# Kernel tuning notes

Hardware: AMD Instinct MI355X
Metric: run time of the kernel (lower is better)

The kernel has to match this reference:

```python
import jax, jax.numpy as jnp
import numpy as np
import math

B, S, D, H = 2048, 32, 1024, 16
DK = D // H
EPS = 1e-5

def setup_inputs() -> dict:
    key = jax.random.key(0)
    ks = jax.random.split(key, 8)
    w_scale = 0.02  # realistic init scale for linear weights
    # Weights stored as (d_in, d_out): y = x @ W + b (same math as torch x @ W.T)
    return {
        "x":  jax.random.normal(ks[0], (B, S, D), jnp.float32),
        "ln_g": jnp.ones((D,), jnp.float32),
        "ln_b": jnp.zeros((D,), jnp.float32),
        "wq": jax.random.normal(ks[1], (D, D), jnp.float32) * w_scale,
        "bq": jnp.zeros((D,), jnp.float32),
        "wk": jax.random.normal(ks[2], (D, D), jnp.float32) * w_scale,
        "bk": jnp.zeros((D,), jnp.float32),
        "wv": jax.random.normal(ks[3], (D, D), jnp.float32) * w_scale,
        "bv": jnp.zeros((D,), jnp.float32),
        "wo": jax.random.normal(ks[4], (D, D), jnp.float32) * w_scale,
        "bo": jnp.zeros((D,), jnp.float32),
        "rel_bias": jax.random.normal(ks[5], (H, 32, 32), jnp.float32),
    }

def reference(x, ln_g, ln_b, wq, bq, wk, bk, wv, bv, wo, bo, rel_bias):
    b, s, d = x.shape
    h = rel_bias.shape[0]
    dk = d // h
    residual = x
    # LayerNorm (eps=1e-5)
    mu = jnp.mean(x, axis=-1, keepdims=True)
    var = jnp.mean(jnp.square(x - mu), axis=-1, keepdims=True)
    xn = (x - mu) * jax.lax.rsqrt(var + EPS) * ln_g + ln_b
    # QKV projections -> [b, h, s, dk]
    def split_heads(t):
        return t.reshape(b, s, h, dk).transpose(0, 2, 1, 3)
    Q = split_heads(xn @ wq + bq)
    K = split_heads(xn @ wk + bk)
    V = split_heads(xn @ wv + bv)
    scores = jnp.einsum('bhqd,bhkd->bhqk', Q, K) / jnp.sqrt(jnp.float32(dk))
    if s <= 32:  # static at trace time, matching the torch branch
        scores = scores + rel_bias[:, :s, :s][None]
    attn = jax.nn.softmax(scores, axis=-1)
    ctx = jnp.einsum('bhqk,bhkd->bhqd', attn, V)
    ctx = ctx.transpose(0, 2, 1, 3).reshape(b, s, d)
    out = ctx @ wo + bo  # dropout is identity in eval
    return residual + out
```

## Files before the change

### kernel.cpp

```cpp
#include <hip/hip_runtime.h>
#include <stdint.h>


typedef __attribute__((ext_vector_type(8))) short bf16x8;
typedef __attribute__((ext_vector_type(4))) float f32x4;
typedef __attribute__((ext_vector_type(16))) float f32x16;

__device__ __forceinline__ float bf2f(unsigned short u) {
    return __uint_as_float(((unsigned)u) << 16);
}
__device__ __forceinline__ unsigned short f2bf(float f) {
    unsigned u = __float_as_uint(f);
    u += 0x7FFFu + ((u >> 16) & 1u);
    return (unsigned short)(u >> 16);
}
__device__ __forceinline__ uint4 pack8(const float* f) {
    uint4 u;
    u.x = (unsigned)f2bf(f[0]) | ((unsigned)f2bf(f[1]) << 16);
    u.y = (unsigned)f2bf(f[2]) | ((unsigned)f2bf(f[3]) << 16);
    u.z = (unsigned)f2bf(f[4]) | ((unsigned)f2bf(f[5]) << 16);
    u.w = (unsigned)f2bf(f[6]) | ((unsigned)f2bf(f[7]) << 16);
    return u;
}

typedef __attribute__((address_space(3))) unsigned lds_u32;
typedef const __attribute__((address_space(1))) unsigned glb_u32;
__device__ __forceinline__ void gld16(const void* g, void* l) {
    __builtin_amdgcn_global_load_lds((glb_u32*)g, (lds_u32*)l, 16, 0, 0);
}

__global__ __launch_bounds__(256) void lnw_kernel(
    const float* __restrict__ x, const float* __restrict__ gg,
    const float* __restrict__ bb, unsigned short* __restrict__ xn,
    const float* __restrict__ wq, const float* __restrict__ wk,
    const float* __restrict__ wv, const float* __restrict__ wo,
    unsigned short* __restrict__ wcatT, unsigned short* __restrict__ woT)
{
    __shared__ unsigned short T[64 * 72];
    if (blockIdx.x >= 16384) {
        int bid = blockIdx.x - 16384;
        int p = bid >> 8;
        int t = bid & 255;
        int k0 = (t >> 4) * 64, n0 = (t & 15) * 64;
        const float* src = (p == 0) ? wq : (p == 1) ? wk : (p == 2) ? wv : wo;
        unsigned short* dst = (p < 3) ? (wcatT + (size_t)p * 1048576) : woT;
        int tid = threadIdx.x;
#pragma unroll
        for (int it = 0; it < 2; it++) {
            int flat = it * 2048 + tid * 8;
            int r = flat >> 6, c = flat & 63;
            const float* s4 = src + (size_t)(k0 + r) * 1024 + n0 + c;
            float4 u0 = *(const float4*)s4;
            float4 u1 = *(const float4*)(s4 + 4);
            float f[8] = {u0.x, u0.y, u0.z, u0.w, u1.x, u1.y, u1.z, u1.w};
            *(uint4*)&T[r * 72 + c] = pack8(f);
        }
        __syncthreads();
#pragma unroll
        for (int it = 0; it < 2; it++) {
            int flat = it * 2048 + tid * 8;
            int rn = flat >> 6, ck = flat & 63;
            unsigned short v[8];
#pragma unroll
            for (int j = 0; j < 8; j++) v[j] = T[(ck + j) * 72 + rn];
            uint4 u;
            u.x = (unsigned)v[0] | ((unsigned)v[1] << 16);
            u.y = (unsigned)v[2] | ((unsigned)v[3] << 16);
            u.z = (unsigned)v[4] | ((unsigned)v[5] << 16);
            u.w = (unsigned)v[6] | ((unsigned)v[7] << 16);
            *(uint4*)(dst + (size_t)(n0 + rn) * 1024 + k0 + ck) = u;
        }
        return;
    }
    int l = threadIdx.x & 63;
    size_t row = (size_t)blockIdx.x * 4 + (threadIdx.x >> 6);
    const float* xr = x + row * 1024;
    float f0[8], f1[8];
    *(float4*)&f0[0] = *(const float4*)(xr + l * 8);
    *(float4*)&f0[4] = *(const float4*)(xr + l * 8 + 4);
    *(float4*)&f1[0] = *(const float4*)(xr + 512 + l * 8);
    *(float4*)&f1[4] = *(const float4*)(xr + 512 + l * 8 + 4);
    float s = 0.f, s2 = 0.f;
#pragma unroll
    for (int j = 0; j < 8; j++) { s += f0[j] + f1[j]; s2 += f0[j] * f0[j] + f1[j] * f1[j]; }
#pragma unroll
    for (int m = 1; m < 64; m <<= 1) { s += __shfl_xor(s, m); s2 += __shfl_xor(s2, m); }
    float mu = s * (1.f / 1024.f);
    float var = s2 * (1.f / 1024.f) - mu * mu;
    float rs = rsqrtf(var + 1e-5f);
    float fg0[8], fg1[8], fb0[8], fb1[8];
    *(float4*)&fg0[0] = *(const float4*)(gg + l * 8);
    *(float4*)&fg0[4] = *(const float4*)(gg + l * 8 + 4);
    *(float4*)&fg1[0] = *(const float4*)(gg + 512 + l * 8);
    *(float4*)&fg1[4] = *(const float4*)(gg + 512 + l * 8 + 4);
    *(float4*)&fb0[0] = *(const float4*)(bb + l * 8);
    *(float4*)&fb0[4] = *(const float4*)(bb + l * 8 + 4);
    *(float4*)&fb1[0] = *(const float4*)(bb + 512 + l * 8);
    *(float4*)&fb1[4] = *(const float4*)(bb + 512 + l * 8 + 4);
    float o0[8], o1[8];
#pragma unroll
    for (int j = 0; j < 8; j++) {
        o0[j] = (f0[j] - mu) * rs * fg0[j] + fb0[j];
        o1[j] = (f1[j] - mu) * rs * fg1[j] + fb1[j];
    }
    *(uint4*)(xn + row * 1024 + l * 8) = pack8(o0);
    *(uint4*)(xn + row * 1024 + 512 + l * 8) = pack8(o1);
}

#define FENCE asm volatile("" ::: "memory")
#define BARRIER do { FENCE; __builtin_amdgcn_s_barrier(); FENCE; } while (0)
#define WAIT_LGKM0 do { asm volatile("s_waitcnt lgkmcnt(0)" ::: "memory"); \
                        __builtin_amdgcn_sched_barrier(0); } while (0)
#define VMCNT(n) asm volatile("s_waitcnt vmcnt(" #n ")" ::: "memory")

#define SAp(buf) (LDSU + (buf) * 16384)
#define SBp(buf) (LDSU + 32768 + (buf) * 16384)

#define STG(gb, hh, kcol, ldsreg) do { \
    const unsigned short* _g = (gb) + (size_t)((hh) * 128) * 1024 + (kcol); \
    unsigned short* _d = (ldsreg) + ((hh) * 128 + w * 8) * 64; \
    gld16(_g, _d); gld16(_g + 64 * 1024, _d + 64 * 64); } while (0)

#define LDA(buf, q, rfq, ks) (*(const bf16x8*)&SAp(buf)[ \
    (wm * 128 + (q) * 32 + (rfq) * 16 + (l & 15)) * 64 + ((((ks) * 32) + khi) ^ aswz)])
#define LDB(buf, cf, ks) (*(const bf16x8*)&SBp(buf)[ \
    (wn * 64 + (cf) * 16 + (l & 15)) * 64 + ((((ks) * 32) + khi) ^ aswz)])

#define MFMA_QUAD(q) do { \
    _Pragma("unroll") \
    for (int cf = 0; cf < 4; cf++) { \
        acc[(q)*2+0][cf] = __builtin_amdgcn_mfma_f32_16x16x32_bf16(aF00, bF[cf][0], acc[(q)*2+0][cf], 0, 0, 0); \
        acc[(q)*2+0][cf] = __builtin_amdgcn_mfma_f32_16x16x32_bf16(aF01, bF[cf][1], acc[(q)*2+0][cf], 0, 0, 0); \
        acc[(q)*2+1][cf] = __builtin_amdgcn_mfma_f32_16x16x32_bf16(aF10, bF[cf][0], acc[(q)*2+1][cf], 0, 0, 0); \
        acc[(q)*2+1][cf] = __builtin_amdgcn_mfma_f32_16x16x32_bf16(aF11, bF[cf][1], acc[(q)*2+1][cf], 0, 0, 0); \
    } } while (0)

#define PHASE(buf, q, STAGE_STMT, TAIL_STMT) do { \
    bf16x8 aF00 = LDA(buf, q, 0, 0), aF01 = LDA(buf, q, 0, 1); \
    bf16x8 aF10 = LDA(buf, q, 1, 0), aF11 = LDA(buf, q, 1, 1); \
    if ((q) == 0) { \
        _Pragma("unroll") \
        for (int cf = 0; cf < 4; cf++) { bF[cf][0] = LDB(buf, cf, 0); bF[cf][1] = LDB(buf, cf, 1); } \
    } \
    STAGE_STMT; \
    BARRIER; \
    WAIT_LGKM0; \
    __builtin_amdgcn_s_setprio(1); \
    MFMA_QUAD(q); \
    __builtin_amdgcn_s_setprio(0); \
    TAIL_STMT; \
    BARRIER; \
} while (0)

template <int MODE>
__global__ __launch_bounds__(512, 2) void gemm8(
    const unsigned short* __restrict__ A, const unsigned short* __restrict__ Bt,
    const float* __restrict__ bz0, const float* __restrict__ bz1,
    const float* __restrict__ bz2, const float* __restrict__ resid,
    void* __restrict__ outv, int NTL, size_t pstride)
{
    __shared__ __align__(16) unsigned short LDSU[65536];
    int cpx = gridDim.x >> 3;
    int bid = (blockIdx.x & 7) * cpx + (blockIdx.x >> 3);
    int mt = bid / NTL, ntl = bid % NTL;
    int m0 = mt * 256, n0 = ntl * 256;
    int tid = threadIdx.x, l = tid & 63, w = tid >> 6;
    int wm = w >> 2, wn = w & 3;
    int khi = (l >> 4) * 8;
    int aswz = (l & 7) * 8;

    const unsigned short* Ag = A + (size_t)(m0 + w * 8 + (l >> 3)) * 1024 + ((l & 7) ^ (l >> 3)) * 8;
    const unsigned short* Bg = Bt + (size_t)(n0 + w * 8 + (l >> 3)) * 1024 + ((l & 7) ^ (l >> 3)) * 8;
    unsigned short* sA0 = SAp(0);
    unsigned short* sA1 = SAp(1);
    unsigned short* sB0 = SBp(0);
    unsigned short* sB1 = SBp(1);

    f32x4 acc[8][4];
#pragma unroll
    for (int i = 0; i < 8; i++)
#pragma unroll
        for (int j = 0; j < 4; j++)
#pragma unroll
            for (int v = 0; v < 4; v++) acc[i][j][v] = 0.f;

    bf16x8 bF[4][2];

    STG(Ag, 0, 0, sA0); STG(Ag, 1, 0, sA0);
    STG(Bg, 0, 0, sB0); STG(Bg, 1, 0, sB0);
    STG(Bg, 0, 64, sB1); STG(Bg, 1, 64, sB1);
    VMCNT(4);
    BARRIER;

    for (int it = 0; it < 7; ++it) {
        int koff = it * 128;
        PHASE(0, 0, STG(Ag, 0, koff + 64, sA1), (void)0);
        PHASE(0, 1, STG(Ag, 1, koff + 64, sA1), (void)0);
        PHASE(0, 2, STG(Bg, 0, koff + 128, sB0), (void)0);
        PHASE(0, 3, STG(Bg, 1, koff + 128, sB0), VMCNT(4));
        PHASE(1, 0, STG(Ag, 0, koff + 128, sA0), (void)0);
        PHASE(1, 1, STG(Ag, 1, koff + 128, sA0), (void)0);
        PHASE(1, 2, STG(Bg, 0, koff + 192, sB1), (void)0);
        PHASE(1, 3, STG(Bg, 1, koff + 192, sB1), VMCNT(4));
    }
    PHASE(0, 0, STG(Ag, 0, 960, sA1), (void)0);
    PHASE(0, 1, STG(Ag, 1, 960, sA1), (void)0);
    PHASE(0, 2, (void)0, (void)0);
    PHASE(0, 3, (void)0, VMCNT(0));
    PHASE(1, 0, (void)0, (void)0);
    PHASE(1, 1, (void)0, (void)0);
    PHASE(1, 2, (void)0, (void)0);
    PHASE(1, 3, (void)0, (void)0);
    __builtin_amdgcn_sched_barrier(0);

    if (MODE == 0) {
        unsigned short* Cs = LDSU;
        unsigned short* out = (unsigned short*)outv;
        int p = n0 >> 10;
        const float* bp = (p == 0) ? bz0 : (p == 1) ? bz1 : bz2;
        size_t pbase = (size_t)p * pstride;
        __syncthreads();
#pragma unroll
        for (int cf = 0; cf < 4; cf++) {
            int colc = wn * 64 + cf * 16 + (l & 15);
            int nn = ((n0 + colc) & 1023);
            float bias = bp[nn];
            int c8 = colc >> 3, ce = colc & 7;
#pragma unroll
            for (int rf = 0; rf < 8; rf++) {
#pragma unroll
                for (int v = 0; v < 4; v++) {
                    int rloc = wm * 128 + rf * 16 + (l >> 4) * 4 + v;
                    Cs[rloc * 256 + ((c8 ^ (rloc & 7)) << 3) + ce] =
                        f2bf(acc[rf][cf][v] + bias);
                }
            }
        }
        __syncthreads();
        int bg0 = m0 >> 5;
        int hg0 = (n0 & 1023) >> 6;
#pragma unroll
        for (int k = 0; k < 4; k++) {
            int pi = w * 4 + k;
            int b = pi >> 2, hh = pi & 3;
#pragma unroll
            for (int r4 = 0; r4 < 4; r4++) {
                int c = r4 * 64 + l;
                int s = c >> 3, d8 = c & 7;
                int row = b * 32 + s;
                int c8 = hh * 8 + d8;
                uint4 val = *(const uint4*)&Cs[row * 256 + ((c8 ^ (row & 7)) << 3)];
                size_t dst = pbase + (((size_t)((bg0 + b) * 16 + hg0 + hh) * 32 + s) << 6) + d8 * 8;
                *(uint4*)(out + dst) = val;
            }
        }
    } else {
        float* Cf = (float*)LDSU;
        float* out = (float*)outv;
        int gcol = n0 + l * 4;
        float4 bzv = *(const float4*)(bz0 + gcol);
#pragma unroll
        for (int pass = 0; pass < 2; pass++) {
            __syncthreads();
#pragma unroll
            for (int rfq = 0; rfq < 4; rfq++) {
                int rf = pass * 4 + rfq;
#pragma unroll
                for (int cf = 0; cf < 4; cf++) {
                    int c0 = wn * 64 + cf * 16 + (l & 15);
                    int c4 = c0 >> 2, ce = c0 & 3;
#pragma unroll
                    for (int v = 0; v < 4; v++) {
                        int rl = wm * 64 + rfq * 16 + (l >> 4) * 4 + v;
                        Cf[rl * 256 + ((c4 ^ (rl & 7)) << 2) + ce] = acc[rf][cf][v];
                    }
                }
            }
            __syncthreads();
#pragma unroll
            for (int rb4 = 0; rb4 < 4; rb4++) {
                float4 rz[4], cv[4];
#pragma unroll
                for (int k = 0; k < 4; k++) {
                    int rr = (rb4 * 4 + k) * 8 + w;
                    int grow = m0 + (rr & 63) + ((rr >> 6) << 7) + pass * 64;
                    rz[k] = *(const float4*)(resid + (size_t)grow * 1024 + gcol);
                }
#pragma unroll
                for (int k = 0; k < 4; k++) {
                    int rr = (rb4 * 4 + k) * 8 + w;
                    cv[k] = *(const float4*)&Cf[rr * 256 + ((l ^ (rr & 7)) << 2)];
                }
#pragma unroll
                for (int k = 0; k < 4; k++) {
                    int rr = (rb4 * 4 + k) * 8 + w;
                    int grow = m0 + (rr & 63) + ((rr >> 6) << 7) + pass * 64;
                    float4 o;
                    o.x = cv[k].x + bzv.x + rz[k].x;
                    o.y = cv[k].y + bzv.y + rz[k].y;
                    o.z = cv[k].z + bzv.z + rz[k].z;
                    o.w = cv[k].w + bzv.w + rz[k].w;
                    *(float4*)(out + (size_t)grow * 1024 + gcol) = o;
                }
            }
        }
    }
}

__global__ __launch_bounds__(512) void attn_kernel(
    const unsigned short* __restrict__ qkv, const float* __restrict__ rb,
    unsigned short* __restrict__ ctx, size_t pstride)
{
    __shared__ unsigned short VT[8][64 * 40];
    __shared__ unsigned short Ps[8][32 * 40];
    int w8 = threadIdx.x >> 6, l = threadIdx.x & 63;
    int col = l & 31, hi = l >> 5;
    int bh = blockIdx.x * 8 + w8, h = bh & 15;
    size_t base = (size_t)bh << 11;
    const unsigned short* Qb = qkv + base;
    const unsigned short* Kb = Qb + pstride;
    const unsigned short* Vb = Kb + pstride;
    unsigned short* vt = VT[w8];
    unsigned short* ps = Ps[w8];

#pragma unroll
    for (int r = 0; r < 4; r++) {
        int flat = r * 512 + l * 8;
        int s = flat >> 6, d0 = flat & 63;
        uint4 u = *(const uint4*)(Vb + flat);
        const unsigned short* e = (const unsigned short*)&u;
#pragma unroll
        for (int j = 0; j < 8; j++) vt[(d0 + j) * 40 + s] = e[j];
    }

    f32x16 acc;
#pragma unroll
    for (int i = 0; i < 16; i++) acc[i] = 0.f;
#pragma unroll
    for (int t = 0; t < 4; t++) {
        bf16x8 aQ = *(const bf16x8*)(Qb + col * 64 + t * 16 + hi * 8);
        bf16x8 bK = *(const bf16x8*)(Kb + col * 64 + t * 16 + hi * 8);
        acc = __builtin_amdgcn_mfma_f32_32x32x16_bf16(aQ, bK, acc, 0, 0, 0);
    }

    const float* rbh = rb + h * 1024;
#pragma unroll
    for (int r = 0; r < 16; r++) {
        int m = (r & 3) + 8 * (r >> 2) + 4 * hi;
        float v = acc[r] * 0.125f + rbh[m * 32 + col];
        float mx = v;
#pragma unroll
        for (int msk = 1; msk < 32; msk <<= 1) mx = fmaxf(mx, __shfl_xor(mx, msk));
        float e = __expf(v - mx);
        float sm = e;
#pragma unroll
        for (int msk = 1; msk < 32; msk <<= 1) sm += __shfl_xor(sm, msk);
        ps[m * 40 + col] = f2bf(e / sm);
    }

    bf16x8 pa0 = *(const bf16x8*)&ps[col * 40 + hi * 8];
    bf16x8 pa1 = *(const bf16x8*)&ps[col * 40 + 16 + hi * 8];
    bf16x8 vb00 = *(const bf16x8*)&vt[(col) * 40 + hi * 8];
    bf16x8 vb01 = *(const bf16x8*)&vt[(col) * 40 + 16 + hi * 8];
    bf16x8 vb10 = *(const bf16x8*)&vt[(32 + col) * 40 + hi * 8];
    bf16x8 vb11 = *(const bf16x8*)&vt[(32 + col) * 40 + 16 + hi * 8];
    f32x16 o0, o1;
#pragma unroll
    for (int i = 0; i < 16; i++) { o0[i] = 0.f; o1[i] = 0.f; }
    o0 = __builtin_amdgcn_mfma_f32_32x32x16_bf16(pa0, vb00, o0, 0, 0, 0);
    o0 = __builtin_amdgcn_mfma_f32_32x32x16_bf16(pa1, vb01, o0, 0, 0, 0);
    o1 = __builtin_amdgcn_mfma_f32_32x32x16_bf16(pa0, vb10, o1, 0, 0, 0);
    o1 = __builtin_amdgcn_mfma_f32_32x32x16_bf16(pa1, vb11, o1, 0, 0, 0);

#pragma unroll
    for (int r = 0; r < 16; r++) {
        int m = (r & 3) + 8 * (r >> 2) + 4 * hi;
        vt[m * 72 + col]      = f2bf(o0[r]);
        vt[m * 72 + 32 + col] = f2bf(o1[r]);
    }
    size_t rowb = (size_t)(bh >> 4) * 32;
#pragma unroll
    for (int pass = 0; pass < 4; pass++) {
        int row = pass * 8 + (l >> 3);
        int c = (l & 7) * 8;
        uint4 val = *(const uint4*)&vt[row * 72 + c];
        *(uint4*)(ctx + (rowb + row) * 1024 + h * 64 + c) = val;
    }
}

extern "C" void kernel_launch(void* const* d_in, const int* in_sizes, int n_in,
                              void* d_out, int out_size, void* d_ws, size_t ws_size,
                              hipStream_t stream)
{
    const float* x  = (const float*)d_in[0];
    const float* lg = (const float*)d_in[1];
    const float* lb = (const float*)d_in[2];
    const float* wq = (const float*)d_in[3];
    const float* bq = (const float*)d_in[4];
    const float* wk = (const float*)d_in[5];
    const float* bk = (const float*)d_in[6];
    const float* wv = (const float*)d_in[7];
    const float* bv = (const float*)d_in[8];
    const float* wo = (const float*)d_in[9];
    const float* bo = (const float*)d_in[10];
    const float* rb = (const float*)d_in[11];
    float* out = (float*)d_out;
    unsigned short* ws = (unsigned short*)d_ws;

    unsigned short* wcatT = ws;
    unsigned short* woT   = wcatT + 3145728;
    unsigned short* xnctx = woT + 1048576;
    unsigned short* qkvc  = xnctx + 67108864ull;

    const size_t elems_fixed = 3145728ull + 1048576ull + 67108864ull;
    const size_t need4 = (elems_fixed + 50331648ull) * 2;
    int nChunks = (ws_size >= need4) ? 4 : 8;
    int rowsPer = 65536 / nChunks;
    size_t pstr = (size_t)rowsPer * 1024;

    lnw_kernel<<<dim3(17408), dim3(256), 0, stream>>>(
        x, lg, lb, xnctx, wq, wk, wv, wo, wcatT, woT);

    int gemm0Grid = (rowsPer / 256) * 12;
    int attnGrid  = rowsPer / 16;

    for (int c = 0; c < nChunks; c++) {
        const unsigned short* Ac = xnctx + (size_t)c * pstr;
        unsigned short* ctxc = xnctx + (size_t)c * pstr;
        gemm8<0><<<dim3(gemm0Grid), dim3(512), 0, stream>>>(
            Ac, wcatT, bq, bk, bv, (const float*)nullptr, (void*)qkvc, 12, pstr);
        attn_kernel<<<dim3(attnGrid), dim3(512), 0, stream>>>(qkvc, rb, ctxc, pstr);
    }

    gemm8<1><<<dim3(1024), dim3(512), 0, stream>>>(
        xnctx, woT, bo, bo, bo, x, (void*)out, 4, 0);
}
```

Measured before the change: 800.7 us.

## Run output projection per chunk and prefetch residual before epilogue repack

The output-projection GEMM now launches inside the chunk loop right after each attention kernel, working on that chunk's context and residual slice instead of one large launch at the end. The aim is to keep the context data hot in cache (L2/LLC) between attention and the projection. The epilogue also loads all 16 residual float4 values per pass into registers before the LDS repack and barrier, so global load latency overlaps with the repack. In exchange there are more, smaller launches with smaller grids per chunk, and the larger residual buffer raises register pressure.

```diff
diff --git a/kernel.cpp b/kernel.cpp
--- a/kernel.cpp
+++ b/kernel.cpp
@@ -152,6 +152,22 @@
     BARRIER; \
 } while (0)
 
+#define REPACK(pass) do { \
+    _Pragma("unroll") \
+    for (int rfq = 0; rfq < 4; rfq++) { \
+        int rf = (pass) * 4 + rfq; \
+        _Pragma("unroll") \
+        for (int cf = 0; cf < 4; cf++) { \
+            int c0 = wn * 64 + cf * 16 + (l & 15); \
+            int c4 = c0 >> 2, ce = c0 & 3; \
+            _Pragma("unroll") \
+            for (int v = 0; v < 4; v++) { \
+                int rl = wm * 64 + rfq * 16 + (l >> 4) * 4 + v; \
+                Cf[rl * 256 + ((c4 ^ (rl & 7)) << 2) + ce] = acc[rf][cf][v]; \
+            } \
+        } \
+    } } while (0)
+
 template <int MODE>
 __global__ __launch_bounds__(512, 2) void gemm8(
     const unsigned short* __restrict__ A, const unsigned short* __restrict__ Bt,
@@ -259,50 +275,49 @@
         float* out = (float*)outv;
         int gcol = n0 + l * 4;
         float4 bzv = *(const float4*)(bz0 + gcol);
-#pragma unroll
-        for (int pass = 0; pass < 2; pass++) {
-            __syncthreads();
-#pragma unroll
-            for (int rfq = 0; rfq < 4; rfq++) {
-                int rf = pass * 4 + rfq;
-#pragma unroll
-                for (int cf = 0; cf < 4; cf++) {
-                    int c0 = wn * 64 + cf * 16 + (l & 15);
-                    int c4 = c0 >> 2, ce = c0 & 3;
-#pragma unroll
-                    for (int v = 0; v < 4; v++) {
-                        int rl = wm * 64 + rfq * 16 + (l >> 4) * 4 + v;
-                        Cf[rl * 256 + ((c4 ^ (rl & 7)) << 2) + ce] = acc[rf][cf][v];
-                    }
-                }
-            }
-            __syncthreads();
-#pragma unroll
-            for (int rb4 = 0; rb4 < 4; rb4++) {
-                float4 rz[4], cv[4];
-#pragma unroll
-                for (int k = 0; k < 4; k++) {
-                    int rr = (rb4 * 4 + k) * 8 + w;
-                    int grow = m0 + (rr & 63) + ((rr >> 6) << 7) + pass * 64;
-                    rz[k] = *(const float4*)(resid + (size_t)grow * 1024 + gcol);
-                }
-#pragma unroll
-                for (int k = 0; k < 4; k++) {
-                    int rr = (rb4 * 4 + k) * 8 + w;
-                    cv[k] = *(const float4*)&Cf[rr * 256 + ((l ^ (rr & 7)) << 2)];
-                }
-#pragma unroll
-                for (int k = 0; k < 4; k++) {
-                    int rr = (rb4 * 4 + k) * 8 + w;
-                    int grow = m0 + (rr & 63) + ((rr >> 6) << 7) + pass * 64;
-                    float4 o;
-                    o.x = cv[k].x + bzv.x + rz[k].x;
-                    o.y = cv[k].y + bzv.y + rz[k].y;
-                    o.z = cv[k].z + bzv.z + rz[k].z;
-                    o.w = cv[k].w + bzv.w + rz[k].w;
-                    *(float4*)(out + (size_t)grow * 1024 + gcol) = o;
-                }
-            }
+
+        float4 rzp[16];
+#pragma unroll
+        for (int k = 0; k < 16; k++) {
+            int rr = k * 8 + w;
+            int grow = m0 + (rr & 63) + ((rr >> 6) << 7);
+            rzp[k] = *(const float4*)(resid + (size_t)grow * 1024 + gcol);
+        }
+        __syncthreads();
+        REPACK(0);
+        __syncthreads();
+#pragma unroll
+        for (int k = 0; k < 16; k++) {
+            int rr = k * 8 + w;
+            int grow = m0 + (rr & 63) + ((rr >> 6) << 7);
+            float4 cv = *(const float4*)&Cf[rr * 256 + ((l ^ (rr & 7)) << 2)];
+            float4 o;
+            o.x = cv.x + bzv.x + rzp[k].x;
+            o.y = cv.y + bzv.y + rzp[k].y;
+            o.z = cv.z + bzv.z + rzp[k].z;
+            o.w = cv.w + bzv.w + rzp[k].w;
+            *(float4*)(out + (size_t)grow * 1024 + gcol) = o;
+        }
+#pragma unroll
+        for (int k = 0; k < 16; k++) {
+            int rr = k * 8 + w;
+            int grow = m0 + (rr & 63) + ((rr >> 6) << 7) + 64;
+            rzp[k] = *(const float4*)(resid + (size_t)grow * 1024 + gcol);
+        }
+        __syncthreads();
+        REPACK(1);
+        __syncthreads();
+#pragma unroll
+        for (int k = 0; k < 16; k++) {
+            int rr = k * 8 + w;
+            int grow = m0 + (rr & 63) + ((rr >> 6) << 7) + 64;
+            float4 cv = *(const float4*)&Cf[rr * 256 + ((l ^ (rr & 7)) << 2)];
+            float4 o;
+            o.x = cv.x + bzv.x + rzp[k].x;
+            o.y = cv.y + bzv.y + rzp[k].y;
+            o.z = cv.z + bzv.z + rzp[k].z;
+            o.w = cv.w + bzv.w + rzp[k].w;
+            *(float4*)(out + (size_t)grow * 1024 + gcol) = o;
         }
     }
 }
@@ -423,6 +438,7 @@
 
     int gemm0Grid = (rowsPer / 256) * 12;
     int attnGrid  = rowsPer / 16;
+    int gemm1Grid = (rowsPer / 256) * 4;
 
     for (int c = 0; c < nChunks; c++) {
         const unsigned short* Ac = xnctx + (size_t)c * pstr;
@@ -430,8 +446,8 @@
         gemm8<0><<<dim3(gemm0Grid), dim3(512), 0, stream>>>(
             Ac, wcatT, bq, bk, bv, (const float*)nullptr, (void*)qkvc, 12, pstr);
         attn_kernel<<<dim3(attnGrid), dim3(512), 0, stream>>>(qkvc, rb, ctxc, pstr);
-    }
-
-    gemm8<1><<<dim3(1024), dim3(512), 0, stream>>>(
-        xnctx, woT, bo, bo, bo, x, (void*)out, 4, 0);
-}
+        gemm8<1><<<dim3(gemm1Grid), dim3(512), 0, stream>>>(
+            ctxc, woT, bo, bo, bo, x + (size_t)c * pstr,
+            (void*)(out + (size_t)c * pstr), 4, 0);
+    }
+}
```

After: 895.4 us. 11.8% more time.
